# Kernel optimization log

Measured on AMD Instinct MI355X. Metric: run time of the kernel, lower is better.

The kernel has to match this reference:

```python
import jax, jax.numpy as jnp
import numpy as np

N, E, G = 100000, 400000, 4096
H, C = 4, 32            # heads, hidden_dim per head
D_OUT = H * C           # 128
NODE_D, EDGE_D = 38, 13
DEC_H, OUT_D = 64, 1
NEG_SLOPE = 0.2
LN_EPS = 1e-5


def setup_inputs() -> dict:
    key = jax.random.key(0)
    ks = jax.random.split(key, 40)
    r = lambda k, s: jax.random.normal(k, s, jnp.float32) * 0.1
    inp = {
        "x": jax.random.normal(ks[0], (N, NODE_D), jnp.float32),
        "edge_index": jax.random.randint(ks[1], (2, E), 0, N),
        "edge_attr": jax.random.uniform(ks[2], (E, EDGE_D), jnp.float32),
        "batch": jnp.sort(jax.random.randint(ks[3], (N,), 0, G)),
        # --- block 1 (in=38) ---
        "Wl1": r(ks[4], (NODE_D, D_OUT)), "bl1": jnp.zeros((D_OUT,), jnp.float32),
        "Wr1": r(ks[5], (NODE_D, D_OUT)), "br1": jnp.zeros((D_OUT,), jnp.float32),
        "We1": r(ks[6], (EDGE_D, D_OUT)),
        "att1": r(ks[7], (H, C)), "ab1": jnp.zeros((D_OUT,), jnp.float32),
        "ln_g1": jnp.ones((D_OUT,), jnp.float32), "ln_b1": jnp.zeros((D_OUT,), jnp.float32),
        "Wres": r(ks[8], (NODE_D, D_OUT)), "bres": jnp.zeros((D_OUT,), jnp.float32),
        # --- block 2 (in=128, residual = identity) ---
        "Wl2": r(ks[9], (D_OUT, D_OUT)), "bl2": jnp.zeros((D_OUT,), jnp.float32),
        "Wr2": r(ks[10], (D_OUT, D_OUT)), "br2": jnp.zeros((D_OUT,), jnp.float32),
        "We2": r(ks[11], (EDGE_D, D_OUT)),
        "att2": r(ks[12], (H, C)), "ab2": jnp.zeros((D_OUT,), jnp.float32),
        "ln_g2": jnp.ones((D_OUT,), jnp.float32), "ln_b2": jnp.zeros((D_OUT,), jnp.float32),
        # --- readout MLP ---
        "Wd1": r(ks[13], (D_OUT, DEC_H)), "bd1": jnp.zeros((DEC_H,), jnp.float32),
        "Wd2": r(ks[14], (DEC_H, OUT_D)), "bd2": jnp.zeros((OUT_D,), jnp.float32),
    }
    return inp


def _segment_softmax(logits, seg, n):
    m = jax.ops.segment_max(logits, seg, num_segments=n)
    ex = jnp.exp(logits - m[seg])
    s = jax.ops.segment_sum(ex, seg, num_segments=n)
    return ex / s[seg]


def _gatv2(x, src, dst, e_feat, Wl, bl, Wr, br, We, att, ab):
    n = x.shape[0]
    xl = (x @ Wl + bl).reshape(n, H, C)   # source transform
    xr = (x @ Wr + br).reshape(n, H, C)   # target transform
    ee = (e_feat @ We).reshape(-1, H, C)  # edge transform
    z = jax.nn.leaky_relu(xl[src] + xr[dst] + ee, NEG_SLOPE)  # [E,H,C]
    logits = jnp.einsum('ehc,hc->eh', z, att)                 # [E,H]
    alpha = _segment_softmax(logits, dst, n)                  # softmax over target nbhd
    out = jax.ops.segment_sum(xl[src] * alpha[..., None], dst, num_segments=n)
    return out.reshape(n, D_OUT) + ab


def _layernorm(h, g, b):
    mu = jnp.mean(h, -1, keepdims=True)
    d = h - mu
    v = jnp.mean(d * d, -1, keepdims=True)
    return d * jax.lax.rsqrt(v + LN_EPS) * g + b


def reference(x, edge_index, edge_attr, batch,
              Wl1, bl1, Wr1, br1, We1, att1, ab1, ln_g1, ln_b1, Wres, bres,
              Wl2, bl2, Wr2, br2, We2, att2, ab2, ln_g2, ln_b2,
              Wd1, bd1, Wd2, bd2):
    src, dst = edge_index[0], edge_index[1]
    n = x.shape[0]
    # add_self_loops(fill_value='mean'): self-loop edge attr = mean of incoming edge attrs
    deg = jax.ops.segment_sum(jnp.ones((src.shape[0],), x.dtype), dst, num_segments=n)
    loop_attr = jax.ops.segment_sum(edge_attr, dst, num_segments=n) / jnp.clip(deg, 1.0)[:, None]
    nodes = jnp.arange(n)
    src_a = jnp.concatenate([src, nodes])
    dst_a = jnp.concatenate([dst, nodes])
    ea = jnp.concatenate([edge_attr, loop_attr], axis=0)

    # block 1
    h = _gatv2(x, src_a, dst_a, ea, Wl1, bl1, Wr1, br1, We1, att1, ab1)
    h = jax.nn.elu(h)
    h = _layernorm(h + (x @ Wres + bres), ln_g1, ln_b1)
    # block 2 (identity residual)
    h2 = _gatv2(h, src_a, dst_a, ea, Wl2, bl2, Wr2, br2, We2, att2, ab2)
    h2 = jax.nn.elu(h2)
    h2 = _layernorm(h2 + h, ln_g2, ln_b2)

    # global mean pool over graphs
    cnt = jax.ops.segment_sum(jnp.ones((n,), x.dtype), batch, num_segments=G)
    g = jax.ops.segment_sum(h2, batch, num_segments=G) / jnp.clip(cnt, 1.0)[:, None]

    return jax.nn.relu(g @ Wd1 + bd1) @ Wd2 + bd2
```

## Files before the change

### kernel.cpp

```cpp
#include <hip/hip_runtime.h>

typedef unsigned short u16;
typedef unsigned int   u32;
typedef __attribute__((ext_vector_type(8))) short short8;
typedef __attribute__((ext_vector_type(4))) float float4v;
typedef __attribute__((ext_vector_type(2))) float float2v;

#define NODE_D   38
#define EDGE_D   13
#define D_OUT    128
#define NEG_SLOPE 0.2f
#define LN_EPS   1e-5f

__device__ __forceinline__ float bf2f(u16 v) { return __uint_as_float(((u32)v) << 16); }
__device__ __forceinline__ u16 f2bf(float f) {
    u32 u = __float_as_uint(f);
    u += 0x7fffu + ((u >> 16) & 1u);
    return (u16)(u >> 16);
}

template <int CTRL>
__device__ __forceinline__ float dpp_radd(float x) {
    int t = __builtin_amdgcn_update_dpp(0, __float_as_int(x), CTRL, 0xf, 0xf, true);
    return x + __int_as_float(t);
}
__device__ __forceinline__ float reduce16(float p) {
    p = dpp_radd<0xB1>(p);
    p = dpp_radd<0x4E>(p);
    p = dpp_radd<0x124>(p);
    p = dpp_radd<0x128>(p);
    return p;
}
__device__ __forceinline__ float reduce64(float v) {
    v = reduce16(v);
    v += __shfl_xor(v, 16, 64);
    v += __shfl_xor(v, 32, 64);
    return v;
}

__global__ void k_pre(const int* __restrict__ dst, int E, int* __restrict__ deg,
                      const int* __restrict__ batch, int N, int G, int* __restrict__ goff,
                      const float* __restrict__ x, u16* __restrict__ xb) {
    int i = blockIdx.x * blockDim.x + threadIdx.x;
    if (i < E) atomicAdd(deg + dst[i], 1);
    if (i < N) {
        int b = batch[i];
        int prev = (i == 0) ? -1 : batch[i - 1];
        for (int g = prev + 1; g <= b; g++) goff[g] = i;
        if (i == N - 1)
            for (int g = b + 1; g <= G; g++) goff[g] = N;
    }
    if (i < N * 32) {
        int n = i >> 5, kk = (i & 31) * 2;
        float f0 = 0.f, f1 = 0.f;
        if (kk < NODE_D) {
            float2v v = *(const float2v*)(x + (size_t)n * NODE_D + kk);
            f0 = v[0]; f1 = v[1];
        }
        ((u32*)xb)[(size_t)n * 32 + (i & 31)] = (u32)f2bf(f0) | ((u32)f2bf(f1) << 16);
    }
}

#define SCAN_CHUNK 1024
__global__ void k_scan1(const int* __restrict__ cnt, int N, int addone, int* __restrict__ bsum) {
    __shared__ int sh[256];
    int base = blockIdx.x * SCAN_CHUNK;
    int t = threadIdx.x;
    int s = 0;
#pragma unroll
    for (int i = 0; i < 4; i++) { int idx = base + t * 4 + i; if (idx < N) s += cnt[idx] + addone; }
    sh[t] = s; __syncthreads();
    for (int ofs = 128; ofs > 0; ofs >>= 1) {
        if (t < ofs) sh[t] += sh[t + ofs];
        __syncthreads();
    }
    if (t == 0) bsum[blockIdx.x] = sh[0];
}
__global__ void k_scan2(const int* __restrict__ bsum, int nb, int* __restrict__ boff) {
    __shared__ int sh[256];
    int t = threadIdx.x;
    if (nb <= 256) {
        int v = (t < nb) ? bsum[t] : 0;
        sh[t] = v; __syncthreads();
        for (int ofs = 1; ofs < 256; ofs <<= 1) {
            int x = (t >= ofs) ? sh[t - ofs] : 0;
            __syncthreads();
            sh[t] += x;
            __syncthreads();
        }
        if (t < nb) boff[t] = sh[t] - v;
        if (t == nb - 1) boff[nb] = sh[t];
    } else if (t == 0) {
        int run = 0;
        for (int i = 0; i < nb; i++) { boff[i] = run; run += bsum[i]; }
        boff[nb] = run;
    }
}
__global__ void k_scan3(const int* __restrict__ cnt, int N, int addone,
                        const int* __restrict__ boff, int nb, int* __restrict__ off) {
    __shared__ int wtot[4];
    int base = blockIdx.x * SCAN_CHUNK;
    int t = threadIdx.x;
    int lane = t & 63, w = t >> 6;
    int v[4]; int s = 0;
#pragma unroll
    for (int i = 0; i < 4; i++) { int idx = base + t * 4 + i; v[i] = (idx < N) ? cnt[idx] + addone : 0; s += v[i]; }
    int inc = s;
#pragma unroll
    for (int ofs = 1; ofs < 64; ofs <<= 1) {
        int x = __shfl_up(inc, ofs, 64);
        if (lane >= ofs) inc += x;
    }
    if (lane == 63) wtot[w] = inc;
    __syncthreads();
    int wofs = 0;
    for (int i = 0; i < w; i++) wofs += wtot[i];
    int run = boff[blockIdx.x] + wofs + (inc - s);
#pragma unroll
    for (int i = 0; i < 4; i++) {
        int idx = base + t * 4 + i;
        if (idx < N) off[idx] = run;
        run += v[i];
    }
    if (blockIdx.x == 0 && t == 0) off[N] = boff[nb];
}

__global__ void k_fill(const int* __restrict__ src, const int* __restrict__ dst,
                       const float* __restrict__ eattr, int E,
                       const int* __restrict__ csr_off, int* __restrict__ fill,
                       int* __restrict__ csr_src, u16* __restrict__ A) {
    int e = blockIdx.x * blockDim.x + threadIdx.x;
    if (e >= E) return;
    int d = dst[e];
    int pos = csr_off[d] + atomicAdd(fill + d, 1);
    csr_src[pos] = src[e];
    u16 row[16];
#pragma unroll
    for (int k = 0; k < EDGE_D; k++) row[k] = f2bf(eattr[(size_t)e * EDGE_D + k]);
#pragma unroll
    for (int k = EDGE_D; k < 16; k++) row[k] = 0;
    uint4* rp = (uint4*)(A + (size_t)pos * 16);
    rp[0] = (uint4){(u32)row[0] | ((u32)row[1] << 16), (u32)row[2] | ((u32)row[3] << 16),
                    (u32)row[4] | ((u32)row[5] << 16), (u32)row[6] | ((u32)row[7] << 16)};
    rp[1] = (uint4){(u32)row[8] | ((u32)row[9] << 16), (u32)row[10] | ((u32)row[11] << 16),
                    (u32)row[12] | ((u32)row[13] << 16), (u32)row[14] | ((u32)row[15] << 16)};
}

__global__ __launch_bounds__(256) void k_self(const int* __restrict__ csr_off, int N,
                                              int* __restrict__ csr_src, u16* __restrict__ A) {
    int wave = blockIdx.x * 4 + (threadIdx.x >> 6);
    if (wave >= N) return;
    int lane = threadIdx.x & 63;
    int r = lane >> 4, k = lane & 15;
    int b = csr_off[wave], e2 = csr_off[wave + 1] - 1;
    float s = 0.f;
    for (int j = b + r; j < e2; j += 4)
        s += bf2f(A[(size_t)j * 16 + k]);
    s += __shfl_xor(s, 16, 64);
    s += __shfl_xor(s, 32, 64);
    if (lane < 16) {
        u16 v = (k < EDGE_D) ? f2bf(s / fmaxf((float)(e2 - b), 1.f)) : (u16)0;
        A[(size_t)e2 * 16 + k] = v;
        if (k == 0) csr_src[e2] = wave;
    }
}

template <int KPAD, int CT, int KREAL, bool IN_BF16>
__global__ __launch_bounds__(256) void k_tf_mfma(
    const void* __restrict__ in_v,
    const float* __restrict__ W0, const float* __restrict__ b0,
    const float* __restrict__ W1, const float* __restrict__ b1,
    const float* __restrict__ W2, const float* __restrict__ b2,
    u16* __restrict__ o0, u16* __restrict__ o1, u16* __restrict__ o2,
    int N) {
    constexpr int RS = KPAD + 8;
    __shared__ u16 Bsw[CT * 16 * RS];
    __shared__ float bsh[CT * 16];
    const float* Ws[3] = {W0, W1, W2};
    const float* bs[3] = {b0, b1, b2};
    u16* outs[3] = {o0, o1, o2};
    int t = threadIdx.x;
    for (int i = t; i < CT * 16 * KPAD; i += 256) {
        int c = i / KPAD, k = i - c * KPAD;
        float v = (k < KREAL) ? Ws[c >> 7][(size_t)k * 128 + (c & 127)] : 0.f;
        Bsw[c * RS + k] = f2bf(v);
    }
    for (int i = t; i < CT * 16; i += 256) bsh[i] = bs[i >> 7][i & 127];
    __syncthreads();

    int wid = t >> 6, lane = t & 63;
    int quad = lane >> 4, m = lane & 15;

    for (int g0 = blockIdx.x * 64; g0 < N; g0 += gridDim.x * 64) {
        int na = g0 + wid * 16 + m;
        if (na > N - 1) na = N - 1;
        short8 a[KPAD / 32];
        if (IN_BF16) {
            const u16* in = (const u16*)in_v;
#pragma unroll
            for (int kc = 0; kc < KPAD / 32; kc++)
                a[kc] = *(const short8*)(in + (size_t)na * KPAD + kc * 32 + quad * 8);
        } else {
            const float* in = (const float*)in_v;
#pragma unroll
            for (int kc = 0; kc < KPAD / 32; kc++)
#pragma unroll
                for (int j = 0; j < 8; j++) {
                    int k = kc * 32 + quad * 8 + j;
                    float v = (k < KREAL) ? in[(size_t)na * KREAL + k] : 0.f;
                    a[kc][j] = (short)f2bf(v);
                }
        }
        float4v acc[CT];
#pragma unroll
        for (int ct = 0; ct < CT; ct++) acc[ct] = (float4v){0.f, 0.f, 0.f, 0.f};
#pragma unroll
        for (int ct = 0; ct < CT; ct++) {
#pragma unroll
            for (int kc = 0; kc < KPAD / 32; kc++) {
                short8 b = *(const short8*)(&Bsw[(ct * 16 + m) * RS + kc * 32 + quad * 8]);
                acc[ct] = __builtin_amdgcn_mfma_f32_16x16x32_bf16(b, a[kc], acc[ct], 0, 0, 0);
            }
        }
        int node = g0 + wid * 16 + m;
        if (node < N) {
#pragma unroll
            for (int ct = 0; ct < CT; ct++) {
                int colb = ct * 16 + quad * 4;
                u16* op = outs[colb >> 7];
                int cc = colb & 127;
                float4v bq = *(const float4v*)&bsh[colb];
                ushort4 wv;
                wv.x = f2bf(acc[ct][0] + bq[0]);
                wv.y = f2bf(acc[ct][1] + bq[1]);
                wv.z = f2bf(acc[ct][2] + bq[2]);
                wv.w = f2bf(acc[ct][3] + bq[3]);
                *(ushort4*)(op + (size_t)node * 128 + cc) = wv;
            }
        }
    }
}

template <bool POOL>
__global__ __launch_bounds__(256) void k_gat(
    const int* __restrict__ csr_off, const int* __restrict__ csr_src,
    const u16* __restrict__ A_csr,
    const u16* __restrict__ xl, const u16* __restrict__ xr,
    const u16* __restrict__ res, const float* __restrict__ We,
    const float* __restrict__ att, const float* __restrict__ ab,
    const float* __restrict__ lng, const float* __restrict__ lnb,
    u16* __restrict__ hout, const int* __restrict__ batch, float* __restrict__ gsum,
    int N, int npw) {
    int t = threadIdx.x;
    int wid = t >> 6, lane = t & 63;
    int wave = blockIdx.x * 4 + wid;
    int n0 = wave * npw;
    if (n0 >= N) return;
    int n1 = n0 + npw; if (n1 > N) n1 = N;

    float2v we2[EDGE_D];
#pragma unroll
    for (int k = 0; k < EDGE_D; k++)
        we2[k] = (float2v){We[k * D_OUT + 2 * lane], We[k * D_OUT + 2 * lane + 1]};
    float a0 = att[2 * lane], a1 = att[2 * lane + 1];
    float abv0 = ab[2 * lane], abv1 = ab[2 * lane + 1];
    float lg0 = lng[2 * lane], lg1 = lng[2 * lane + 1];
    float lb0 = lnb[2 * lane], lb1 = lnb[2 * lane + 1];

    const u32* xl32 = (const u32*)xl;
    const u32* xr32 = (const u32*)xr;
    int wbeg = csr_off[n0];
    int wend = csr_off[n1];
    int nedge = wend - wbeg;

    float ps0 = 0.f, ps1 = 0.f;
    int gcur = POOL ? batch[n0] : -1;

    auto finish = [&](int n, float ssum, float2v acc2) {
        float inv = 1.f / ssum;
        float o0 = acc2[0] * inv + abv0;
        float o1 = acc2[1] * inv + abv1;
        o0 = (o0 > 0.f) ? o0 : (__expf(o0) - 1.f);
        o1 = (o1 > 0.f) ? o1 : (__expf(o1) - 1.f);
        u32 rw = ((const u32*)res)[(size_t)n * 64 + lane];
        o0 += bf2f((u16)(rw & 0xffff));
        o1 += bf2f((u16)(rw >> 16));
        float sm = reduce64(o0 + o1);
        float mu = sm * (1.f / 128.f);
        float d0 = o0 - mu, d1 = o1 - mu;
        float vv = reduce64(d0 * d0 + d1 * d1);
        float rs = rsqrtf(vv * (1.f / 128.f) + LN_EPS);
        float h0 = d0 * rs * lg0 + lb0;
        float h1 = d1 * rs * lg1 + lb1;
        if (POOL) {
            int g = batch[n];
            if (g != gcur) {
                atomicAdd(gsum + (size_t)gcur * 128 + 2 * lane, ps0);
                atomicAdd(gsum + (size_t)gcur * 128 + 2 * lane + 1, ps1);
                ps0 = 0.f; ps1 = 0.f; gcur = g;
            }
            ps0 += h0; ps1 += h1;
        } else {
            ((u32*)hout)[(size_t)n * 64 + lane] = (u32)f2bf(h0) | ((u32)f2bf(h1) << 16);
        }
    };

    const float2v z0v = (float2v){0.f, 0.f};

    if (nedge <= 64) {
        int last = nedge - 1;
        int sv = csr_src[wbeg + ((lane < nedge) ? lane : last)];
        int f0 = __builtin_amdgcn_readlane(sv, 0);
        int f1 = __builtin_amdgcn_readlane(sv, (1 <= last) ? 1 : last);
        int f2 = __builtin_amdgcn_readlane(sv, (2 <= last) ? 2 : last);
        int f3 = __builtin_amdgcn_readlane(sv, (3 <= last) ? 3 : last);
        u32 xw0 = xl32[(size_t)f0 * 64 + lane];
        u32 xw1 = xl32[(size_t)f1 * 64 + lane];
        u32 xw2 = xl32[(size_t)f2 * 64 + lane];
        u32 xw3 = xl32[(size_t)f3 * 64 + lane];
        int wbu = __builtin_amdgcn_readfirstlane(wbeg);
        const uint4* ap = (const uint4*)(A_csr + (size_t)wbu * 16);
        uint4 aq0 = ap[0], aq1 = ap[1];

        int i = wbeg;
        for (int n = n0; n < n1; n++) {
            int end = csr_off[n + 1];
            u32 xrw = xr32[(size_t)n * 64 + lane];
            float2v xr2 = (float2v){bf2f((u16)(xrw & 0xffff)), bf2f((u16)(xrw >> 16))};
            float ssum = 0.f;
            float2v acc2 = (float2v){0.f, 0.f};
            for (; i < end; i++) {
                int j4 = i + 4 - wbeg; if (j4 > last) j4 = last;
                int f4 = __builtin_amdgcn_readlane(sv, j4);
                u32 xwN = xl32[(size_t)f4 * 64 + lane];
                int j1n = i + 1 - wbeg; if (j1n > last) j1n = last;
                int ipu = __builtin_amdgcn_readfirstlane(wbeg + j1n);
                const uint4* apn = (const uint4*)(A_csr + (size_t)ipu * 16);
                uint4 an0 = apn[0], an1 = apn[1];

                u32 dw[8] = {aq0.x, aq0.y, aq0.z, aq0.w, aq1.x, aq1.y, aq1.z, aq1.w};
                float2v eeA = (float2v){0.f, 0.f}, eeB = (float2v){0.f, 0.f};
#pragma unroll
                for (int k = 0; k < EDGE_D; k++) {
                    u32 d = dw[k >> 1];
                    float av = __uint_as_float((k & 1) ? (d & 0xffff0000u) : (d << 16));
                    if ((k >> 1) & 1) eeB += we2[k] * av;
                    else             eeA += we2[k] * av;
                }
                float2v xs = (float2v){bf2f((u16)(xw0 & 0xffff)), bf2f((u16)(xw0 >> 16))};
                float2v z = (xs + xr2) + (eeA + eeB);
                float2v lz = __builtin_elementwise_max(z, z0v) + __builtin_elementwise_min(z, z0v) * NEG_SLOPE;
                float p = lz[0] * a0 + lz[1] * a1;
                p = reduce16(p);
                float wgt = __expf(p);
                ssum += wgt;
                acc2 += xs * wgt;
                xw0 = xw1; xw1 = xw2; xw2 = xw3; xw3 = xwN;
                aq0 = an0; aq1 = an1;
            }
            finish(n, ssum, acc2);
        }
    } else {
        int cl = wend - 1;
        int f = csr_src[wbeg];
        u32 xw = xl32[(size_t)f * 64 + lane];
        int wbu = __builtin_amdgcn_readfirstlane(wbeg);
        const uint4* ap = (const uint4*)(A_csr + (size_t)wbu * 16);
        uint4 aq0 = ap[0], aq1 = ap[1];
        int i = wbeg;
        for (int n = n0; n < n1; n++) {
            int end = csr_off[n + 1];
            u32 xrw = xr32[(size_t)n * 64 + lane];
            float2v xr2 = (float2v){bf2f((u16)(xrw & 0xffff)), bf2f((u16)(xrw >> 16))};
            float ssum = 0.f;
            float2v acc2 = (float2v){0.f, 0.f};
            for (; i < end; i++) {
                u32 xwc = xw; uint4 q0 = aq0, q1 = aq1;
                int ip = (i + 1 < wend) ? i + 1 : cl;
                f = csr_src[ip];
                xw = xl32[(size_t)f * 64 + lane];
                int ipu = __builtin_amdgcn_readfirstlane(ip);
                const uint4* ap2 = (const uint4*)(A_csr + (size_t)ipu * 16);
                aq0 = ap2[0]; aq1 = ap2[1];
                u32 dw[8] = {q0.x, q0.y, q0.z, q0.w, q1.x, q1.y, q1.z, q1.w};
                float2v eeA = (float2v){0.f, 0.f}, eeB = (float2v){0.f, 0.f};
#pragma unroll
                for (int k = 0; k < EDGE_D; k++) {
                    u32 d = dw[k >> 1];
                    float av = __uint_as_float((k & 1) ? (d & 0xffff0000u) : (d << 16));
                    if ((k >> 1) & 1) eeB += we2[k] * av;
                    else             eeA += we2[k] * av;
                }
                float2v xs = (float2v){bf2f((u16)(xwc & 0xffff)), bf2f((u16)(xwc >> 16))};
                float2v z = (xs + xr2) + (eeA + eeB);
                float2v lz = __builtin_elementwise_max(z, z0v) + __builtin_elementwise_min(z, z0v) * NEG_SLOPE;
                float p = lz[0] * a0 + lz[1] * a1;
                p = reduce16(p);
                float wgt = __expf(p);
                ssum += wgt;
                acc2 += xs * wgt;
            }
            finish(n, ssum, acc2);
        }
    }

    if (POOL) {
        atomicAdd(gsum + (size_t)gcur * 128 + 2 * lane, ps0);
        atomicAdd(gsum + (size_t)gcur * 128 + 2 * lane + 1, ps1);
    }
}

__global__ __launch_bounds__(128) void k_read(
    const float* __restrict__ gsum, const int* __restrict__ goff,
    const float* __restrict__ Wd1, const float* __restrict__ bd1,
    const float* __restrict__ Wd2, const float* __restrict__ bd2,
    float* __restrict__ out, int G) {
    __shared__ float psh[128];
    __shared__ float rsh[2][64];
    int g = blockIdx.x;
    int t = threadIdx.x;
    int cnt = goff[g + 1] - goff[g];
    float inv = 1.f / fmaxf((float)cnt, 1.f);
    psh[t] = gsum[(size_t)g * 128 + t] * inv;
    __syncthreads();
    int j = t & 63, hw = t >> 6;
    float acc = (hw == 0) ? bd1[j] : 0.f;
    int k0 = hw * 64;
    for (int k = k0; k < k0 + 64; k++)
        acc += psh[k] * Wd1[k * 64 + j];
    rsh[hw][j] = acc;
    __syncthreads();
    if (t < 64) {
        float a = fmaxf(rsh[0][t] + rsh[1][t], 0.f);
        float v = a * Wd2[t];
#pragma unroll
        for (int mk = 1; mk < 64; mk <<= 1) v += __shfl_xor(v, mk, 64);
        if (t == 0) out[g] = v + bd2[0];
    }
}

extern "C" void kernel_launch(void* const* d_in, const int* in_sizes, int n_in,
                              void* d_out, int out_size, void* d_ws, size_t ws_size,
                              hipStream_t stream) {
    const float* x     = (const float*)d_in[0];
    const int*   eidx  = (const int*)d_in[1];
    const float* eattr = (const float*)d_in[2];
    const int*   batch = (const int*)d_in[3];
    const float* Wl1 = (const float*)d_in[4],  *bl1 = (const float*)d_in[5];
    const float* Wr1 = (const float*)d_in[6],  *br1 = (const float*)d_in[7];
    const float* We1 = (const float*)d_in[8],  *att1 = (const float*)d_in[9],  *ab1 = (const float*)d_in[10];
    const float* lng1 = (const float*)d_in[11], *lnb1 = (const float*)d_in[12];
    const float* Wres = (const float*)d_in[13], *bres = (const float*)d_in[14];
    const float* Wl2 = (const float*)d_in[15], *bl2 = (const float*)d_in[16];
    const float* Wr2 = (const float*)d_in[17], *br2 = (const float*)d_in[18];
    const float* We2 = (const float*)d_in[19], *att2 = (const float*)d_in[20], *ab2 = (const float*)d_in[21];
    const float* lng2 = (const float*)d_in[22], *lnb2 = (const float*)d_in[23];
    const float* Wd1 = (const float*)d_in[24], *bd1 = (const float*)d_in[25];
    const float* Wd2 = (const float*)d_in[26], *bd2 = (const float*)d_in[27];

    int N = in_sizes[0] / NODE_D;
    int E = in_sizes[1] / 2;
    int G = out_size;
    int EN = E + N;
    const int* src = eidx;
    const int* dst = eidx + E;

    char* w = (char*)d_ws;
    auto alloc = [&](size_t bytes) -> char* {
        char* p = w;
        w += (bytes + 255) & ~(size_t)255;
        return p;
    };
    int NB = (N + SCAN_CHUNK - 1) / SCAN_CHUNK;
    int*   csr_off  = (int*)alloc((size_t)(N + 1) * 4);
    int*   csr_src  = (int*)alloc((size_t)EN * 4);
    u16*   A_csr    = (u16*)alloc((size_t)(EN + 64) * 16 * 2);
    u16*   xb       = (u16*)alloc((size_t)N * 64 * 2);
    u16*   xlb      = (u16*)alloc((size_t)N * D_OUT * 2);
    u16*   xrb      = (u16*)alloc((size_t)N * D_OUT * 2);
    u16*   resb     = (u16*)alloc((size_t)N * D_OUT * 2);
    u16*   hb       = (u16*)alloc((size_t)N * D_OUT * 2);
    int*   goff     = (int*)alloc((size_t)(G + 1) * 4);
    size_t szN = ((size_t)N * 4 + 255) & ~(size_t)255;
    size_t szG = ((size_t)G * 128 * 4 + 255) & ~(size_t)255;
    char*  zp   = alloc(2 * szN + szG);
    int*   deg  = (int*)zp;
    int*   fill = (int*)(zp + szN);
    float* gsum = (float*)(zp + 2 * szN);
    int*   bsum = (int*)alloc((size_t)(NB + 1) * 4);
    int*   boff = (int*)alloc((size_t)(NB + 1) * 4);

    hipMemsetAsync(zp, 0, 2 * szN + szG, stream);

    int mx = (E > N * 32) ? E : N * 32;
    k_pre<<<(mx + 255) / 256, 256, 0, stream>>>(dst, E, deg, batch, N, G, goff, x, xb);

    k_scan1<<<NB, 256, 0, stream>>>(deg, N, 1, bsum);
    k_scan2<<<1, 256, 0, stream>>>(bsum, NB, boff);
    k_scan3<<<NB, 256, 0, stream>>>(deg, N, 1, boff, NB, csr_off);
    k_fill<<<(E + 255) / 256, 256, 0, stream>>>(src, dst, eattr, E, csr_off, fill, csr_src, A_csr);
    k_self<<<(N + 3) / 4, 256, 0, stream>>>(csr_off, N, csr_src, A_csr);

    int npw = 4;
    int gblocks = (N + npw * 4 - 1) / (npw * 4);

    k_tf_mfma<64, 24, NODE_D, true><<<512, 256, 0, stream>>>(
        xb, Wl1, bl1, Wr1, br1, Wres, bres, xlb, xrb, resb, N);
    k_gat<false><<<gblocks, 256, 0, stream>>>(csr_off, csr_src, A_csr,
                                              xlb, xrb, resb, We1, att1, ab1, lng1, lnb1,
                                              hb, nullptr, nullptr, N, npw);

    k_tf_mfma<128, 16, 128, true><<<512, 256, 0, stream>>>(
        hb, Wl2, bl2, Wr2, br2, Wr2, br2, xlb, xrb, xrb, N);
    k_gat<true><<<gblocks, 256, 0, stream>>>(csr_off, csr_src, A_csr,
                                             xlb, xrb, hb, We2, att2, ab2, lng2, lnb2,
                                             (u16*)nullptr, batch, gsum, N, npw);

    k_read<<<G, 128, 0, stream>>>(gsum, goff, Wd1, bd1, Wd2, bd2, (float*)d_out, G);
}
```

Baseline: 540.0 us.

## Compute block-1 target and residual transforms inside GAT kernel from node input

The first-layer target (xr) and residual projections are no longer produced by the MFMA transform kernel and stored as bf16 arrays. The GAT kernel loads Wr1 and Wres into shared memory and computes both per destination node from the 38-dim bf16 input row. This removes two N×128 bf16 writes and their reads, and shrinks the first transform to only Wl1. In exchange the GAT kernel does extra scalar FMAs per node, adds an LDS staging step with a block barrier, and uses more registers.

Result: slower. 633.9 us (+17.4%).

```diff
diff --git a/kernel.cpp b/kernel.cpp
--- a/kernel.cpp
+++ b/kernel.cpp
@@ -241,18 +241,33 @@
     }
 }
 
-template <bool POOL>
+template <bool XRRES, bool POOL>
 __global__ __launch_bounds__(256) void k_gat(
     const int* __restrict__ csr_off, const int* __restrict__ csr_src,
     const u16* __restrict__ A_csr,
     const u16* __restrict__ xl, const u16* __restrict__ xr,
-    const u16* __restrict__ res, const float* __restrict__ We,
+    const u16* __restrict__ res, const u16* __restrict__ xbin,
+    const float* __restrict__ We,
     const float* __restrict__ att, const float* __restrict__ ab,
     const float* __restrict__ lng, const float* __restrict__ lnb,
+    const float* __restrict__ Wr, const float* __restrict__ brp,
+    const float* __restrict__ Wrs, const float* __restrict__ brs,
     u16* __restrict__ hout, const int* __restrict__ batch, float* __restrict__ gsum,
     int N, int npw) {
     int t = threadIdx.x;
     int wid = t >> 6, lane = t & 63;
+
+    __shared__ float2v wlds[XRRES ? 2 * NODE_D * 64 : 1];
+    if (XRRES) {
+        for (int i = t; i < 2 * NODE_D * 64; i += 256) {
+            int row = i >> 6, l = i & 63;
+            const float* Wsrc = (row < NODE_D) ? Wr : Wrs;
+            int k = (row < NODE_D) ? row : row - NODE_D;
+            wlds[row * 64 + l] = *(const float2v*)(Wsrc + (size_t)k * 128 + 2 * l);
+        }
+        __syncthreads();
+    }
+
     int wave = blockIdx.x * 4 + wid;
     int n0 = wave * npw;
     if (n0 >= N) return;
@@ -266,9 +281,15 @@
     float abv0 = ab[2 * lane], abv1 = ab[2 * lane + 1];
     float lg0 = lng[2 * lane], lg1 = lng[2 * lane + 1];
     float lb0 = lnb[2 * lane], lb1 = lnb[2 * lane + 1];
+    float brv0 = 0.f, brv1 = 0.f, bsv0 = 0.f, bsv1 = 0.f;
+    if (XRRES) {
+        brv0 = brp[2 * lane]; brv1 = brp[2 * lane + 1];
+        bsv0 = brs[2 * lane]; bsv1 = brs[2 * lane + 1];
+    }
 
     const u32* xl32 = (const u32*)xl;
     const u32* xr32 = (const u32*)xr;
+    const u32* xb32 = (const u32*)xbin;
     int wbeg = csr_off[n0];
     int wend = csr_off[n1];
     int nedge = wend - wbeg;
@@ -276,15 +297,43 @@
     float ps0 = 0.f, ps1 = 0.f;
     int gcur = POOL ? batch[n0] : -1;
 
-    auto finish = [&](int n, float ssum, float2v acc2) {
+    auto node_pre = [&](int n, float2v& xr2, float2v& rs2) {
+        if (XRRES) {
+            int nu = __builtin_amdgcn_readfirstlane(n);
+            const u32* xrow = xb32 + (size_t)nu * 32;
+            xr2 = (float2v){brv0, brv1};
+            rs2 = (float2v){bsv0, bsv1};
+#pragma unroll
+            for (int k2 = 0; k2 < NODE_D / 2; k2++) {
+                u32 xw = xrow[k2];
+                float xk0 = bf2f((u16)(xw & 0xffff));
+                float xk1 = bf2f((u16)(xw >> 16));
+                int k = 2 * k2;
+                xr2 += wlds[k * 64 + lane] * xk0;
+                xr2 += wlds[(k + 1) * 64 + lane] * xk1;
+                rs2 += wlds[(NODE_D + k) * 64 + lane] * xk0;
+                rs2 += wlds[(NODE_D + k + 1) * 64 + lane] * xk1;
+            }
+        } else {
+            u32 xrw = xr32[(size_t)n * 64 + lane];
+            xr2 = (float2v){bf2f((u16)(xrw & 0xffff)), bf2f((u16)(xrw >> 16))};
+            rs2 = (float2v){0.f, 0.f};
+        }
+    };
+
+    auto finish = [&](int n, float ssum, float2v acc2, float2v rs2) {
         float inv = 1.f / ssum;
         float o0 = acc2[0] * inv + abv0;
         float o1 = acc2[1] * inv + abv1;
         o0 = (o0 > 0.f) ? o0 : (__expf(o0) - 1.f);
         o1 = (o1 > 0.f) ? o1 : (__expf(o1) - 1.f);
-        u32 rw = ((const u32*)res)[(size_t)n * 64 + lane];
-        o0 += bf2f((u16)(rw & 0xffff));
-        o1 += bf2f((u16)(rw >> 16));
+        if (XRRES) {
+            o0 += rs2[0]; o1 += rs2[1];
+        } else {
+            u32 rw = ((const u32*)res)[(size_t)n * 64 + lane];
+            o0 += bf2f((u16)(rw & 0xffff));
+            o1 += bf2f((u16)(rw >> 16));
+        }
         float sm = reduce64(o0 + o1);
         float mu = sm * (1.f / 128.f);
         float d0 = o0 - mu, d1 = o1 - mu;
@@ -325,8 +374,8 @@
         int i = wbeg;
         for (int n = n0; n < n1; n++) {
             int end = csr_off[n + 1];
-            u32 xrw = xr32[(size_t)n * 64 + lane];
-            float2v xr2 = (float2v){bf2f((u16)(xrw & 0xffff)), bf2f((u16)(xrw >> 16))};
+            float2v xr2, rs2;
+            node_pre(n, xr2, rs2);
             float ssum = 0.f;
             float2v acc2 = (float2v){0.f, 0.f};
             for (; i < end; i++) {
@@ -358,7 +407,7 @@
                 xw0 = xw1; xw1 = xw2; xw2 = xw3; xw3 = xwN;
                 aq0 = an0; aq1 = an1;
             }
-            finish(n, ssum, acc2);
+            finish(n, ssum, acc2, rs2);
         }
     } else {
         int cl = wend - 1;
@@ -370,8 +419,8 @@
         int i = wbeg;
         for (int n = n0; n < n1; n++) {
             int end = csr_off[n + 1];
-            u32 xrw = xr32[(size_t)n * 64 + lane];
-            float2v xr2 = (float2v){bf2f((u16)(xrw & 0xffff)), bf2f((u16)(xrw >> 16))};
+            float2v xr2, rs2;
+            node_pre(n, xr2, rs2);
             float ssum = 0.f;
             float2v acc2 = (float2v){0.f, 0.f};
             for (; i < end; i++) {
@@ -400,7 +449,7 @@
                 ssum += wgt;
                 acc2 += xs * wgt;
             }
-            finish(n, ssum, acc2);
+            finish(n, ssum, acc2, rs2);
         }
     }
 
@@ -478,7 +527,6 @@
     u16*   xb       = (u16*)alloc((size_t)N * 64 * 2);
     u16*   xlb      = (u16*)alloc((size_t)N * D_OUT * 2);
     u16*   xrb      = (u16*)alloc((size_t)N * D_OUT * 2);
-    u16*   resb     = (u16*)alloc((size_t)N * D_OUT * 2);
     u16*   hb       = (u16*)alloc((size_t)N * D_OUT * 2);
     int*   goff     = (int*)alloc((size_t)(G + 1) * 4);
     size_t szN = ((size_t)N * 4 + 255) & ~(size_t)255;
@@ -504,17 +552,19 @@
     int npw = 4;
     int gblocks = (N + npw * 4 - 1) / (npw * 4);
 
-    k_tf_mfma<64, 24, NODE_D, true><<<512, 256, 0, stream>>>(
-        xb, Wl1, bl1, Wr1, br1, Wres, bres, xlb, xrb, resb, N);
-    k_gat<false><<<gblocks, 256, 0, stream>>>(csr_off, csr_src, A_csr,
-                                              xlb, xrb, resb, We1, att1, ab1, lng1, lnb1,
-                                              hb, nullptr, nullptr, N, npw);
+    k_tf_mfma<64, 8, NODE_D, true><<<784, 256, 0, stream>>>(
+        xb, Wl1, bl1, Wl1, bl1, Wl1, bl1, xlb, xlb, xlb, N);
+    k_gat<true, false><<<gblocks, 256, 0, stream>>>(
+        csr_off, csr_src, A_csr, xlb, nullptr, nullptr, xb,
+        We1, att1, ab1, lng1, lnb1, Wr1, br1, Wres, bres,
+        hb, nullptr, nullptr, N, npw);
 
     k_tf_mfma<128, 16, 128, true><<<512, 256, 0, stream>>>(
         hb, Wl2, bl2, Wr2, br2, Wr2, br2, xlb, xrb, xrb, N);
-    k_gat<true><<<gblocks, 256, 0, stream>>>(csr_off, csr_src, A_csr,
-                                             xlb, xrb, hb, We2, att2, ab2, lng2, lnb2,
-                                             (u16*)nullptr, batch, gsum, N, npw);
+    k_gat<false, true><<<gblocks, 256, 0, stream>>>(
+        csr_off, csr_src, A_csr, xlb, xrb, hb, nullptr,
+        We2, att2, ab2, lng2, lnb2, nullptr, nullptr, nullptr, nullptr,
+        (u16*)nullptr, batch, gsum, N, npw);
 
     k_read<<<G, 128, 0, stream>>>(gsum, goff, Wd1, bd1, Wd2, bd2, (float*)d_out, G);
 }
```
